# Performance work log

Hardware: AMD Instinct MI355X
Metric: run time of the kernel (lower is better)

Reference implementation:

```python
import jax, jax.numpy as jnp
import numpy as np

SIGMA = 0.02          # walker step std
CORR_LEN = 10         # correlation_length
N = 65536             # n_samples (walkers)
NE = 16               # n_elec
D = NE * 3            # flattened coord dim
H = 256               # surrogate MLP hidden


def setup_inputs() -> dict:
    key = jax.random.key(0)
    ks = jax.random.split(key, 6)
    return {
        "curr_sample": jax.random.normal(ks[0], (N, NE, 3), jnp.float32),
        "W1": jax.random.normal(ks[1], (D, H), jnp.float32) * 0.1,
        "b1": jnp.zeros((H,), jnp.float32),
        "w2": jax.random.normal(ks[2], (H,), jnp.float32) * 0.1,
        "Wh": jax.random.normal(ks[3], (D, H), jnp.float32) * 0.1,
        "bh": jnp.zeros((H,), jnp.float32),
        "wh2": jax.random.normal(ks[4], (H,), jnp.float32) * 0.1,
    }


def _log_amp(x, W, b, w):
    # x: [n, NE, 3] -> scalar log-amplitude per walker: [n]
    f = x.reshape(x.shape[0], -1)
    return jnp.tanh(f @ W + b) @ w


def reference(curr_sample, W1, b1, w2, Wh, bh, wh2):
    n = curr_sample.shape[0]
    half = n // 2
    sm = curr_sample[:half]   # model-sampled walkers
    sh = curr_sample[half:]   # HF-sampled walkers
    # to_prob(log_amp) = exp(log_amp)**2 = exp(2*log_amp)
    pm = jnp.exp(2.0 * _log_amp(sm, W1, b1, w2))
    ph = jnp.exp(2.0 * _log_amp(sh, Wh, bh, wh2))

    step_keys = jax.random.split(jax.random.key(42), CORR_LEN)

    def step(carry, k):
        sm, pm, sh, ph = carry
        k1, k2, k3, k4 = jax.random.split(k, 4)
        new_sm = sm + SIGMA * jax.random.normal(k1, sm.shape, sm.dtype)
        new_pm = jnp.exp(2.0 * _log_amp(new_sm, W1, b1, w2))
        new_sh = sh + SIGMA * jax.random.normal(k2, sh.shape, sh.dtype)
        new_ph = jnp.exp(2.0 * _log_amp(new_sh, Wh, bh, wh2))
        mm = (new_pm / pm) > jax.random.uniform(k3, (half,), sm.dtype)
        mh = (new_ph / ph) > jax.random.uniform(k4, (half,), sh.dtype)
        sm = jnp.where(mm[:, None, None], new_sm, sm)
        pm = jnp.where(mm, new_pm, pm)
        sh = jnp.where(mh[:, None, None], new_sh, sh)
        ph = jnp.where(mh, new_ph, ph)
        return (sm, pm, sh, ph), None

    (sm, pm, sh, ph), _ = jax.lax.scan(step, (sm, pm, sh, ph), step_keys)
    out = jnp.concatenate([sm, sh], axis=0)
    perm = jax.random.permutation(jax.random.key(7), n)  # torch.randperm analog
    return out[perm]
```

## Files before the change

kernel.cpp:

```cpp
#include <hip/hip_runtime.h>
#include <cstdint>
#include <cstring>
#include <vector>
#include <numeric>
#include <algorithm>


typedef __attribute__((ext_vector_type(2))) float f32x2;
typedef __attribute__((ext_vector_type(4))) float f32x4;

static constexpr int kHalfN = 32768;
static constexpr int kSteps = 10;
static constexpr int kD = 48;
static constexpr int kH = 256;
static constexpr int kS = 8;
static constexpr int kWPB = 8;
static constexpr int kXW = kD * kS;

struct StepKeys {
  uint32_t kn[2][kSteps][2];
  uint32_t ku[2][kSteps][2];
};

__host__ __device__ __forceinline__ void tf2x32(uint32_t k0, uint32_t k1,
                                                uint32_t x0, uint32_t x1,
                                                uint32_t& y0, uint32_t& y1) {
  const uint32_t ks2 = k0 ^ k1 ^ 0x1BD11BDAu;
  x0 += k0; x1 += k1;
#define TFR(r) do { x0 += x1; x1 = (x1 << (r)) | (x1 >> (32 - (r))); x1 ^= x0; } while (0)
  TFR(13); TFR(15); TFR(26); TFR(6);
  x0 += k1;  x1 += ks2 + 1u;
  TFR(17); TFR(29); TFR(16); TFR(24);
  x0 += ks2; x1 += k0 + 2u;
  TFR(13); TFR(15); TFR(26); TFR(6);
  x0 += k0;  x1 += k1 + 3u;
  TFR(17); TFR(29); TFR(16); TFR(24);
  x0 += k1;  x1 += ks2 + 4u;
  TFR(13); TFR(15); TFR(26); TFR(6);
  x0 += ks2; x1 += k0 + 5u;
#undef TFR
  y0 = x0; y1 = x1;
}

__device__ __forceinline__ uint32_t tf_xor(uint32_t k0, uint32_t k1, uint32_t i) {
  uint32_t a, b;
  tf2x32(k0, k1, 0u, i, a, b);
  return a ^ b;
}

__device__ __forceinline__ float unit_from_bits(uint32_t bits) {
  return __uint_as_float((bits >> 9) | 0x3F800000u) - 1.0f;
}

__device__ __forceinline__ float normal_from_bits(uint32_t bits) {
  const float f  = unit_from_bits(bits);
  const float lo = __uint_as_float(0xBF7FFFFFu);
  float u = __fadd_rn(__fmul_rn(f, 2.0f), lo);
  u = fmaxf(u, lo);
  const float uu = __fmul_rn(u, u);
  float w = -__logf(1.0f - uu);
  float wc = w - 2.5f;
  float p = 2.81022636e-08f;
  p = fmaf(p, wc, 3.43273939e-07f);
  p = fmaf(p, wc, -3.5233877e-06f);
  p = fmaf(p, wc, -4.39150654e-06f);
  p = fmaf(p, wc, 0.00021858087f);
  p = fmaf(p, wc, -0.00125372503f);
  p = fmaf(p, wc, -0.00417768164f);
  p = fmaf(p, wc, 0.246640727f);
  p = fmaf(p, wc, 1.50140941f);
  if (__any(w >= 5.0f)) {
    float wt = sqrtf(w) - 3.0f;
    float q = -0.000200214257f;
    q = fmaf(q, wt, 0.000100950558f);
    q = fmaf(q, wt, 0.00134934322f);
    q = fmaf(q, wt, -0.00367342844f);
    q = fmaf(q, wt, 0.00573950773f);
    q = fmaf(q, wt, -0.0076224613f);
    q = fmaf(q, wt, 0.00943887047f);
    q = fmaf(q, wt, 1.00167406f);
    q = fmaf(q, wt, 2.83297682f);
    p = (w < 5.0f) ? p : q;
  }
  return __fmul_rn(__uint_as_float(0x3FB504F3u), __fmul_rn(p, u));
}

__device__ __forceinline__ float readlane_f(float v, int l) {
  return __int_as_float(__builtin_amdgcn_readlane(__float_as_int(v), l));
}

__device__ __forceinline__ float fast_tanh(float x) {
  const float xc = fminf(x, 44.0f);
  const float t = __expf(xc + xc);
  const float a = t + 1.0f;
  float r = __builtin_amdgcn_rcpf(a);
  r = r * (2.0f - a * r);
  return fmaf(-2.0f, r, 1.0f);
}

__device__ __forceinline__ float wave_sum64(float v) {
  v += __int_as_float(__builtin_amdgcn_ds_swizzle(__float_as_int(v), 0x041F));
  v += __int_as_float(__builtin_amdgcn_ds_swizzle(__float_as_int(v), 0x081F));
  v += __int_as_float(__builtin_amdgcn_ds_swizzle(__float_as_int(v), 0x101F));
  v += __int_as_float(__builtin_amdgcn_ds_swizzle(__float_as_int(v), 0x201F));
  v += __int_as_float(__builtin_amdgcn_ds_swizzle(__float_as_int(v), 0x401F));
  v += __shfl_xor(v, 32);
  return v;
}

__device__ __forceinline__ void mlpS(const float* __restrict__ sW,
                                     const float* __restrict__ sX,
                                     int lane,
                                     const float breg[4], const float wreg[4],
                                     float p[kS]) {
  f32x2 acc[4][4];
#pragma unroll
  for (int sp = 0; sp < 4; ++sp)
#pragma unroll
    for (int m = 0; m < 4; ++m) acc[sp][m] = (f32x2){0.f, 0.f};
  const float* wp = sW + (lane << 2);
#pragma unroll 4
  for (int d = 0; d < kD; ++d) {
    const f32x4 w4 = *reinterpret_cast<const f32x4*>(wp + (d << 8));
    const f32x2 w01 = __builtin_shufflevector(w4, w4, 0, 1);
    const f32x2 w23 = __builtin_shufflevector(w4, w4, 2, 3);
    const float* xr = sX + (d << 3);
    const f32x4 xa = *reinterpret_cast<const f32x4*>(xr);
    const f32x4 xb = *reinterpret_cast<const f32x4*>(xr + 4);
    f32x2 f2[4];
    f2[0] = __builtin_shufflevector(xa, xa, 0, 1);
    f2[1] = __builtin_shufflevector(xa, xa, 2, 3);
    f2[2] = __builtin_shufflevector(xb, xb, 0, 1);
    f2[3] = __builtin_shufflevector(xb, xb, 2, 3);
#pragma unroll
    for (int sp = 0; sp < 4; ++sp) {
      asm("v_pk_fma_f32 %0, %1, %2, %0 op_sel_hi:[0,1,1]"
          : "+v"(acc[sp][0]) : "v"(w01), "v"(f2[sp]));
      asm("v_pk_fma_f32 %0, %1, %2, %0 op_sel:[1,0,0] op_sel_hi:[1,1,1]"
          : "+v"(acc[sp][1]) : "v"(w01), "v"(f2[sp]));
      asm("v_pk_fma_f32 %0, %1, %2, %0 op_sel_hi:[0,1,1]"
          : "+v"(acc[sp][2]) : "v"(w23), "v"(f2[sp]));
      asm("v_pk_fma_f32 %0, %1, %2, %0 op_sel:[1,0,0] op_sel_hi:[1,1,1]"
          : "+v"(acc[sp][3]) : "v"(w23), "v"(f2[sp]));
    }
  }
#pragma unroll
  for (int s = 0; s < kS; ++s) {
    const int sp = s >> 1, h = s & 1;
    float pv = 0.f;
#pragma unroll
    for (int m = 0; m < 4; ++m)
      pv = fmaf(fast_tanh(acc[sp][m][h] + breg[m]), wreg[m], pv);
    p[s] = wave_sum64(pv);
  }
}

__device__ __forceinline__ void writeX(float* __restrict__ sX, int lane,
                                       const float v[kS]) {
  if (lane < kD) {
    float* xr = sX + (lane << 3);
#pragma unroll
    for (int sp = 0; sp < 4; ++sp) {
      f32x2 t = {v[2 * sp], v[2 * sp + 1]};
      *reinterpret_cast<f32x2*>(xr + 2 * sp) = t;
    }
  }
}

__global__ __launch_bounds__(512, 2) void mh_chain_kernel(
    const float* __restrict__ curr,
    const float* __restrict__ W1, const float* __restrict__ b1, const float* __restrict__ w2,
    const float* __restrict__ Wh, const float* __restrict__ bh, const float* __restrict__ wh2,
    const uint32_t* __restrict__ iperm,
    float* __restrict__ out,
    StepKeys keys)
{
  __shared__ float sW[kD * kH];
  __shared__ float sX[kWPB * kXW];
  const int bid  = (int)blockIdx.x;
  const int half = bid >> 9;
  const float* W    = half ? Wh  : W1;
  const float* bsrc = half ? bh  : b1;
  const float* wsrc = half ? wh2 : w2;

  for (int j = (int)threadIdx.x; j < kD * kH; j += 512) {
    const int d = j >> 8, cc = j & 255;
    sW[j] = W[(d << 8) | ((cc >> 2) | ((cc & 3) << 6))];
  }
  __syncthreads();

  const int wv   = (int)(threadIdx.x >> 6);
  const int lane = (int)(threadIdx.x & 63);
  float* xw = sX + wv * kXW;
  const int base    = ((bid & 511) << 6) | (wv << 3);
  const int rowBase = half * kHalfN + base;

  float breg[4], wreg[4];
#pragma unroll
  for (int m = 0; m < 4; ++m) {
    breg[m] = bsrc[lane + 64 * m];
    wreg[m] = wsrc[lane + 64 * m];
  }

  float sv[kS];
#pragma unroll
  for (int s = 0; s < kS; ++s)
    sv[s] = (lane < kD) ? curr[(rowBase + s) * kD + lane] : 0.f;

  writeX(xw, lane, sv);
  float p0[kS];
  mlpS(sW, xw, lane, breg, wreg, p0);
  float pc[kS];
#pragma unroll
  for (int s = 0; s < kS; ++s) pc[s] = __expf(__fmul_rn(2.0f, p0[s]));

#pragma unroll 1
  for (int t = 0; t < kSteps; ++t) {
    const uint32_t kn0 = keys.kn[half][t][0], kn1 = keys.kn[half][t][1];
    const uint32_t ku0 = keys.ku[half][t][0], ku1 = keys.ku[half][t][1];

    float uvv, nw[kS];
    {
      const bool noiser = lane < kD;
      const uint32_t k0 = noiser ? kn0 : ku0;
      const uint32_t k1 = noiser ? kn1 : ku1;
      const uint32_t ctr = noiser ? (uint32_t)(base * kD + lane)
                                  : (uint32_t)(base + lane - 48);
      const uint32_t bits = tf_xor(k0, k1, ctr);
      const float nv = normal_from_bits(bits);
      uvv = unit_from_bits(bits);
      nw[0] = __fadd_rn(sv[0], __fmul_rn(0.02f, nv));
    }
#pragma unroll
    for (int s = 1; s < kS; ++s) {
      const uint32_t bits = tf_xor(kn0, kn1, (uint32_t)((base + s) * kD + lane));
      nw[s] = __fadd_rn(sv[s], __fmul_rn(0.02f, normal_from_bits(bits)));
    }

    writeX(xw, lane, nw);
    float pn[kS];
    mlpS(sW, xw, lane, breg, wreg, pn);
#pragma unroll
    for (int s = 0; s < kS; ++s) {
      const float e = __expf(__fmul_rn(2.0f, pn[s]));
      const float us = readlane_f(uvv, 48 + s);
      const bool ok = e > __fmul_rn(us, pc[s]);
      sv[s] = ok ? nw[s] : sv[s];
      pc[s] = ok ? e : pc[s];
    }
  }

#pragma unroll
  for (int s = 0; s < kS; ++s) {
    const int dst = (int)iperm[rowBase + s];
    if (lane < kD) out[dst * kD + lane] = sv[s];
  }
}

struct HostInit {
  StepKeys keys;
  uint32_t iperm[65536];
  HostInit() {
    const uint32_t k42_0 = 0u, k42_1 = 42u;
    for (int t = 0; t < kSteps; ++t) {
      uint32_t sk0, sk1;
      tf2x32(k42_0, k42_1, 0u, (uint32_t)t, sk0, sk1);
      uint32_t k[4][2];
      for (int j = 0; j < 4; ++j) tf2x32(sk0, sk1, 0u, (uint32_t)j, k[j][0], k[j][1]);
      keys.kn[0][t][0] = k[0][0]; keys.kn[0][t][1] = k[0][1];
      keys.kn[1][t][0] = k[1][0]; keys.kn[1][t][1] = k[1][1];
      keys.ku[0][t][0] = k[2][0]; keys.ku[0][t][1] = k[2][1];
      keys.ku[1][t][0] = k[3][0]; keys.ku[1][t][1] = k[3][1];
    }
    const int n = 65536;
    uint32_t kc0 = 0u, kc1 = 7u;
    std::vector<uint32_t> bits(n), val(n), idx(n), nv(n);
    std::iota(val.begin(), val.end(), 0u);
    for (int r = 0; r < 2; ++r) {
      uint32_t nk0, nk1, sub0, sub1;
      tf2x32(kc0, kc1, 0u, 0u, nk0, nk1);
      tf2x32(kc0, kc1, 0u, 1u, sub0, sub1);
      kc0 = nk0; kc1 = nk1;
      for (int i = 0; i < n; ++i) {
        uint32_t a, b;
        tf2x32(sub0, sub1, 0u, (uint32_t)i, a, b);
        bits[i] = a ^ b;
      }
      std::iota(idx.begin(), idx.end(), 0u);
      std::stable_sort(idx.begin(), idx.end(),
                       [&](uint32_t x, uint32_t y) { return bits[x] < bits[y]; });
      for (int i = 0; i < n; ++i) nv[i] = val[idx[i]];
      val.swap(nv);
    }
    for (int i = 0; i < n; ++i) iperm[val[i]] = (uint32_t)i;
  }
};
static const HostInit g_init;

extern "C" void kernel_launch(void* const* d_in, const int* in_sizes, int n_in,
                              void* d_out, int out_size, void* d_ws, size_t ws_size,
                              hipStream_t stream) {
  (void)in_sizes; (void)n_in; (void)out_size; (void)ws_size;
  const float* curr = (const float*)d_in[0];
  const float* W1   = (const float*)d_in[1];
  const float* b1   = (const float*)d_in[2];
  const float* w2   = (const float*)d_in[3];
  const float* Wh   = (const float*)d_in[4];
  const float* bh   = (const float*)d_in[5];
  const float* wh2  = (const float*)d_in[6];
  float* out = (float*)d_out;

  hipMemcpyAsync(d_ws, g_init.iperm, sizeof(g_init.iperm),
                 hipMemcpyHostToDevice, stream);

  mh_chain_kernel<<<dim3(1024), dim3(512), 0, stream>>>(
      curr, W1, b1, w2, Wh, bh, wh2, (const uint32_t*)d_ws, out, g_init.keys);
}
```

Baseline: 427.0 us.

## Compute surrogate MLP with split-bf16 MFMA and 16 walkers per wave

Replaces the packed-FP32 FMA hidden-layer matmul with bf16 MFMA instructions. Both weights and inputs are split into high and low bf16 parts, and all four cross products are accumulated to approximate FP32 accuracy. Weights are pre-swizzled into an MFMA-friendly shared-memory layout. Each wave now handles 16 walkers instead of 8, so the grid is halved. This is meant to move the dominant matmul work off the vector ALUs. The risk is small numerical differences from the bf16 split, which could flip borderline Metropolis acceptances.

```diff
diff --git a/kernel.cpp b/kernel.cpp
--- a/kernel.cpp
+++ b/kernel.cpp
@@ -8,14 +8,15 @@
 
 typedef __attribute__((ext_vector_type(2))) float f32x2;
 typedef __attribute__((ext_vector_type(4))) float f32x4;
+typedef __attribute__((ext_vector_type(8))) short bf16x8;
 
 static constexpr int kHalfN = 32768;
 static constexpr int kSteps = 10;
 static constexpr int kD = 48;
 static constexpr int kH = 256;
-static constexpr int kS = 8;
+static constexpr int kS = 16;
 static constexpr int kWPB = 8;
-static constexpr int kXW = kD * kS;
+static constexpr int kXPitch = 52;
 
 struct StepKeys {
   uint32_t kn[2][kSteps][2];
@@ -98,73 +99,101 @@
   return fmaf(-2.0f, r, 1.0f);
 }
 
-__device__ __forceinline__ float wave_sum64(float v) {
-  v += __int_as_float(__builtin_amdgcn_ds_swizzle(__float_as_int(v), 0x041F));
-  v += __int_as_float(__builtin_amdgcn_ds_swizzle(__float_as_int(v), 0x081F));
-  v += __int_as_float(__builtin_amdgcn_ds_swizzle(__float_as_int(v), 0x101F));
-  v += __int_as_float(__builtin_amdgcn_ds_swizzle(__float_as_int(v), 0x201F));
-  v += __int_as_float(__builtin_amdgcn_ds_swizzle(__float_as_int(v), 0x401F));
-  v += __shfl_xor(v, 32);
-  return v;
-}
-
-__device__ __forceinline__ void mlpS(const float* __restrict__ sW,
-                                     const float* __restrict__ sX,
-                                     int lane,
-                                     const float breg[4], const float wreg[4],
-                                     float p[kS]) {
-  f32x2 acc[4][4];
-#pragma unroll
-  for (int sp = 0; sp < 4; ++sp)
-#pragma unroll
-    for (int m = 0; m < 4; ++m) acc[sp][m] = (f32x2){0.f, 0.f};
-  const float* wp = sW + (lane << 2);
-#pragma unroll 4
-  for (int d = 0; d < kD; ++d) {
-    const f32x4 w4 = *reinterpret_cast<const f32x4*>(wp + (d << 8));
-    const f32x2 w01 = __builtin_shufflevector(w4, w4, 0, 1);
-    const f32x2 w23 = __builtin_shufflevector(w4, w4, 2, 3);
-    const float* xr = sX + (d << 3);
-    const f32x4 xa = *reinterpret_cast<const f32x4*>(xr);
-    const f32x4 xb = *reinterpret_cast<const f32x4*>(xr + 4);
-    f32x2 f2[4];
-    f2[0] = __builtin_shufflevector(xa, xa, 0, 1);
-    f2[1] = __builtin_shufflevector(xa, xa, 2, 3);
-    f2[2] = __builtin_shufflevector(xb, xb, 0, 1);
-    f2[3] = __builtin_shufflevector(xb, xb, 2, 3);
-#pragma unroll
-    for (int sp = 0; sp < 4; ++sp) {
-      asm("v_pk_fma_f32 %0, %1, %2, %0 op_sel_hi:[0,1,1]"
-          : "+v"(acc[sp][0]) : "v"(w01), "v"(f2[sp]));
-      asm("v_pk_fma_f32 %0, %1, %2, %0 op_sel:[1,0,0] op_sel_hi:[1,1,1]"
-          : "+v"(acc[sp][1]) : "v"(w01), "v"(f2[sp]));
-      asm("v_pk_fma_f32 %0, %1, %2, %0 op_sel_hi:[0,1,1]"
-          : "+v"(acc[sp][2]) : "v"(w23), "v"(f2[sp]));
-      asm("v_pk_fma_f32 %0, %1, %2, %0 op_sel:[1,0,0] op_sel_hi:[1,1,1]"
-          : "+v"(acc[sp][3]) : "v"(w23), "v"(f2[sp]));
-    }
-  }
-#pragma unroll
-  for (int s = 0; s < kS; ++s) {
-    const int sp = s >> 1, h = s & 1;
-    float pv = 0.f;
-#pragma unroll
-    for (int m = 0; m < 4; ++m)
-      pv = fmaf(fast_tanh(acc[sp][m][h] + breg[m]), wreg[m], pv);
-    p[s] = wave_sum64(pv);
-  }
-}
-
-__device__ __forceinline__ void writeX(float* __restrict__ sX, int lane,
-                                       const float v[kS]) {
-  if (lane < kD) {
-    float* xr = sX + (lane << 3);
-#pragma unroll
-    for (int sp = 0; sp < 4; ++sp) {
-      f32x2 t = {v[2 * sp], v[2 * sp + 1]};
-      *reinterpret_cast<f32x2*>(xr + 2 * sp) = t;
-    }
-  }
+__device__ __forceinline__ uint32_t bf16_rne_u(uint32_t u) {
+  return (u + 0x7FFFu + ((u >> 16) & 1u)) >> 16;
+}
+
+union FragCast { uint32_t u[4]; bf16x8 v; };
+
+__device__ __forceinline__ uint32_t cvtpk(float a, float b) {
+  uint32_t r;
+  asm("v_cvt_pk_bf16_f32 %0, %1, %2" : "=v"(r) : "v"(a), "v"(b));
+  return r;
+}
+
+#define SWZ_ADD(X, P) \
+  (X) += __int_as_float(__builtin_amdgcn_ds_swizzle(__float_as_int(X), (P)))
+
+__device__ __forceinline__ void evalMLP(const unsigned short* __restrict__ sB,
+                                        const float* __restrict__ xw,
+                                        int smp, int q, int fo0, int fo1,
+                                        const float breg[16], const float wreg[16],
+                                        f32x4& partOut) {
+  const float* xrow = xw + smp * kXPitch;
+  const f32x4 xa = *reinterpret_cast<const f32x4*>(xrow + q * 8);
+  const f32x4 xb = *reinterpret_cast<const f32x4*>(xrow + q * 8 + 4);
+  const int d1 = 32 + (q & 1) * 8;
+  const f32x4 xc = *reinterpret_cast<const f32x4*>(xrow + d1);
+  const f32x4 xd = *reinterpret_cast<const f32x4*>(xrow + d1 + 4);
+
+  FragCast Ahi0, Alo0, Ahi1, Alo1;
+#pragma unroll
+  for (int j = 0; j < 2; ++j) {
+    {
+      float a = xa[2 * j], b = xa[2 * j + 1];
+      uint32_t h = cvtpk(a, b);
+      float la = a - __uint_as_float(h << 16);
+      float lb = b - __uint_as_float(h & 0xFFFF0000u);
+      Ahi0.u[j] = h; Alo0.u[j] = cvtpk(la, lb);
+    }
+    {
+      float a = xb[2 * j], b = xb[2 * j + 1];
+      uint32_t h = cvtpk(a, b);
+      float la = a - __uint_as_float(h << 16);
+      float lb = b - __uint_as_float(h & 0xFFFF0000u);
+      Ahi0.u[2 + j] = h; Alo0.u[2 + j] = cvtpk(la, lb);
+    }
+    {
+      float a = xc[2 * j], b = xc[2 * j + 1];
+      uint32_t h = cvtpk(a, b);
+      float la = a - __uint_as_float(h << 16);
+      float lb = b - __uint_as_float(h & 0xFFFF0000u);
+      Ahi1.u[j] = h; Alo1.u[j] = cvtpk(la, lb);
+    }
+    {
+      float a = xd[2 * j], b = xd[2 * j + 1];
+      uint32_t h = cvtpk(a, b);
+      float la = a - __uint_as_float(h << 16);
+      float lb = b - __uint_as_float(h & 0xFFFF0000u);
+      Ahi1.u[2 + j] = h; Alo1.u[2 + j] = cvtpk(la, lb);
+    }
+  }
+  const uint32_t msk = (q < 2) ? 0xFFFFFFFFu : 0u;
+#pragma unroll
+  for (int j = 0; j < 4; ++j) { Ahi1.u[j] &= msk; Alo1.u[j] &= msk; }
+
+  f32x4 part = {0.f, 0.f, 0.f, 0.f};
+#pragma unroll
+  for (int t = 0; t < 16; ++t) {
+    const bf16x8 bh0 = *reinterpret_cast<const bf16x8*>(sB + t * 768 + fo0);
+    const bf16x8 bh1 = *reinterpret_cast<const bf16x8*>(sB + t * 768 + fo1);
+    const bf16x8 bl0 = *reinterpret_cast<const bf16x8*>(sB + 12288 + t * 768 + fo0);
+    const bf16x8 bl1 = *reinterpret_cast<const bf16x8*>(sB + 12288 + t * 768 + fo1);
+    f32x4 c0 = {0.f, 0.f, 0.f, 0.f};
+    f32x4 c1 = {0.f, 0.f, 0.f, 0.f};
+    c0 = __builtin_amdgcn_mfma_f32_16x16x32_bf16(Ahi0.v, bh0, c0, 0, 0, 0);
+    c1 = __builtin_amdgcn_mfma_f32_16x16x32_bf16(Alo0.v, bh0, c1, 0, 0, 0);
+    c0 = __builtin_amdgcn_mfma_f32_16x16x32_bf16(Ahi1.v, bh1, c0, 0, 0, 0);
+    c1 = __builtin_amdgcn_mfma_f32_16x16x32_bf16(Alo1.v, bh1, c1, 0, 0, 0);
+    c0 = __builtin_amdgcn_mfma_f32_16x16x32_bf16(Ahi0.v, bl0, c0, 0, 0, 0);
+    c1 = __builtin_amdgcn_mfma_f32_16x16x32_bf16(Alo0.v, bl0, c1, 0, 0, 0);
+    c0 = __builtin_amdgcn_mfma_f32_16x16x32_bf16(Ahi1.v, bl1, c0, 0, 0, 0);
+    c1 = __builtin_amdgcn_mfma_f32_16x16x32_bf16(Alo1.v, bl1, c1, 0, 0, 0);
+#pragma unroll
+    for (int r = 0; r < 4; ++r) {
+      const float v = (c0[r] + c1[r]) + breg[t];
+      part[r] = fmaf(fast_tanh(v), wreg[t], part[r]);
+    }
+  }
+#pragma unroll
+  for (int r = 0; r < 4; ++r) SWZ_ADD(part[r], 0x041F);
+#pragma unroll
+  for (int r = 0; r < 4; ++r) SWZ_ADD(part[r], 0x081F);
+#pragma unroll
+  for (int r = 0; r < 4; ++r) SWZ_ADD(part[r], 0x101F);
+#pragma unroll
+  for (int r = 0; r < 4; ++r) SWZ_ADD(part[r], 0x201F);
+  partOut = part;
 }
 
 __global__ __launch_bounds__(512, 2) void mh_chain_kernel(
@@ -175,44 +204,60 @@
     float* __restrict__ out,
     StepKeys keys)
 {
-  __shared__ float sW[kD * kH];
-  __shared__ float sX[kWPB * kXW];
+  __shared__ unsigned short sB[2 * 12288];
+  __shared__ __align__(16) float sX[kWPB * kS * kXPitch];
   const int bid  = (int)blockIdx.x;
-  const int half = bid >> 9;
+  const int half = bid >= 256;
   const float* W    = half ? Wh  : W1;
   const float* bsrc = half ? bh  : b1;
   const float* wsrc = half ? wh2 : w2;
 
-  for (int j = (int)threadIdx.x; j < kD * kH; j += 512) {
-    const int d = j >> 8, cc = j & 255;
-    sW[j] = W[(d << 8) | ((cc >> 2) | ((cc & 3) << 6))];
+  for (int i = (int)threadIdx.x; i < kD * kH; i += 512) {
+    const int d = i >> 8, h = i & 255;
+    const float w = W[i];
+    const uint32_t hb = bf16_rne_u(__float_as_uint(w));
+    const float lof = w - __uint_as_float(hb << 16);
+    const uint32_t lb = bf16_rne_u(__float_as_uint(lof));
+    const int t = h >> 4, c = h & 15, s = d >> 5, kl = d & 31;
+    const int idx = t * 768 + s * 512 + (((kl >> 3) << 4) | c) * 8 + (kl & 7);
+    sB[idx] = (unsigned short)hb;
+    sB[12288 + idx] = (unsigned short)lb;
   }
   __syncthreads();
 
   const int wv   = (int)(threadIdx.x >> 6);
   const int lane = (int)(threadIdx.x & 63);
-  float* xw = sX + wv * kXW;
-  const int base    = ((bid & 511) << 6) | (wv << 3);
+  const int smp  = lane & 15;
+  const int q    = lane >> 4;
+  float* xw = sX + wv * (kS * kXPitch);
+  const int base    = ((bid & 255) << 7) | (wv << 4);
   const int rowBase = half * kHalfN + base;
 
-  float breg[4], wreg[4];
-#pragma unroll
-  for (int m = 0; m < 4; ++m) {
-    breg[m] = bsrc[lane + 64 * m];
-    wreg[m] = wsrc[lane + 64 * m];
+  const int fo0 = lane * 8;
+  const int fo1 = (lane < 32) ? (512 + lane * 8) : (lane * 8);
+
+  float breg[16], wreg[16];
+#pragma unroll
+  for (int t = 0; t < 16; ++t) {
+    breg[t] = bsrc[t * 16 + smp];
+    wreg[t] = wsrc[t * 16 + smp];
   }
 
   float sv[kS];
 #pragma unroll
   for (int s = 0; s < kS; ++s)
     sv[s] = (lane < kD) ? curr[(rowBase + s) * kD + lane] : 0.f;
-
-  writeX(xw, lane, sv);
-  float p0[kS];
-  mlpS(sW, xw, lane, breg, wreg, p0);
+  if (lane < kD) {
+#pragma unroll
+    for (int s = 0; s < kS; ++s) xw[s * kXPitch + lane] = sv[s];
+  }
+
+  f32x4 part;
+  evalMLP(sB, xw, smp, q, fo0, fo1, breg, wreg, part);
   float pc[kS];
 #pragma unroll
-  for (int s = 0; s < kS; ++s) pc[s] = __expf(__fmul_rn(2.0f, p0[s]));
+  for (int s = 0; s < kS; ++s)
+    pc[s] = __expf(__fmul_rn(2.0f, readlane_f(part[s & 3], (s >> 2) << 4)));
 
 #pragma unroll 1
   for (int t = 0; t < kSteps; ++t) {
@@ -237,12 +282,16 @@
       nw[s] = __fadd_rn(sv[s], __fmul_rn(0.02f, normal_from_bits(bits)));
     }
 
-    writeX(xw, lane, nw);
-    float pn[kS];
-    mlpS(sW, xw, lane, breg, wreg, pn);
+    if (lane < kD) {
+#pragma unroll
+      for (int s = 0; s < kS; ++s) xw[s * kXPitch + lane] = nw[s];
+    }
+    f32x4 pn;
+    evalMLP(sB, xw, smp, q, fo0, fo1, breg, wreg, pn);
 #pragma unroll
     for (int s = 0; s < kS; ++s) {
-      const float e = __expf(__fmul_rn(2.0f, pn[s]));
+      const float la = readlane_f(pn[s & 3], (s >> 2) << 4);
+      const float e = __expf(__fmul_rn(2.0f, la));
       const float us = readlane_f(uvv, 48 + s);
       const bool ok = e > __fmul_rn(us, pc[s]);
       sv[s] = ok ? nw[s] : sv[s];
@@ -310,9 +359,9 @@
   const float* wh2  = (const float*)d_in[6];
   float* out = (float*)d_out;
 
-  hipMemcpyAsync(d_ws, g_init.iperm, sizeof(g_init.iperm),
-                 hipMemcpyHostToDevice, stream);
-
-  mh_chain_kernel<<<dim3(1024), dim3(512), 0, stream>>>(
+  (void)hipMemcpyAsync(d_ws, g_init.iperm, sizeof(g_init.iperm),
+                       hipMemcpyHostToDevice, stream);
+
+  mh_chain_kernel<<<dim3(512), dim3(512), 0, stream>>>(
       curr, W1, b1, w2, Wh, bh, wh2, (const uint32_t*)d_ws, out, g_init.keys);
 }
```

Result: slower. 530.6 us (+24.2%).
